# Optimization experiments

Hardware: AMD Instinct MI355X
Metric: run time of the kernel (lower is better)

## Reference

```python
import jax, jax.numpy as jnp
import numpy as np

TOP_K = 128
HID = 256


def _mlp2(h, w1, b1, w2, b2):
    return jax.nn.relu(h @ w1 + b1) @ w2 + b2


def setup_inputs() -> dict:
    key = jax.random.key(0)
    ks = jax.random.split(key, 20)
    B, L, D = 512, 256, 64
    s = 0.05
    inp = {
        "x": jax.random.normal(ks[0], (B, L, D), dtype=jnp.float32),
        "Wq": jax.random.normal(ks[1], (D, HID)) * s, "bq": jnp.zeros((HID,)),
        "Wk": jax.random.normal(ks[2], (D, HID)) * s, "bk": jnp.zeros((HID,)),
        "phi_w1": jax.random.normal(ks[3], (D, HID)) * s, "phi_b1": jnp.zeros((HID,)),
        "phi_w2": jax.random.normal(ks[4], (HID, HID)) * s, "phi_b2": jnp.zeros((HID,)),
        "xi_w1": jax.random.normal(ks[5], (2 * D, HID)) * s, "xi_b1": jnp.zeros((HID,)),
        "xi_w2": jax.random.normal(ks[6], (HID, HID)) * s, "xi_b2": jnp.zeros((HID,)),
        "rho_w1": jax.random.normal(ks[7], (HID, HID)) * s, "rho_b1": jnp.zeros((HID,)),
        "rho_w2": jax.random.normal(ks[8], (HID, 128)) * s, "rho_b2": jnp.zeros((128,)),
    }
    return inp


def reference(x, Wq, bq, Wk, bk, phi_w1, phi_b1, phi_w2, phi_b2,
              xi_w1, xi_b1, xi_w2, xi_b2, rho_w1, rho_b1, rho_w2, rho_b2):
    B, L, D = x.shape
    scale = HID ** (-0.5)
    # padding mask (all True for randn input; trim is identity with static shapes)
    pad = jnp.sum(jnp.abs(x), axis=-1) != 0  # [B, L]
    Q = x @ Wq + bq  # [B, L, H]
    K = x @ Wk + bk
    scores = jnp.einsum("blh,bmh->blm", Q, K) * scale  # [B, L, L]
    mask2d = pad[:, :, None] & pad[:, None, :]
    scores = jnp.where(mask2d, scores, -jnp.inf)
    flat = scores.reshape(B, L * L)
    k = min(TOP_K, L * L)
    topk_vals, topk_idx = jax.lax.top_k(flat, k)  # [B, k]
    topk_w = jax.nn.softmax(topk_vals, axis=-1)
    row = topk_idx // L
    col = topk_idx % L
    x_i = jnp.take_along_axis(x, row[:, :, None], axis=1)  # [B, k, D]
    x_j = jnp.take_along_axis(x, col[:, :, None], axis=1)
    feat_self = _mlp2(x_i, phi_w1, phi_b1, phi_w2, phi_b2)  # [B, k, H]
    feat_pair = _mlp2(jnp.concatenate([x_i, x_j], axis=-1), xi_w1, xi_b1, xi_w2, xi_b2)
    self_mask = (row == col)[:, :, None]
    interaction = jnp.where(self_mask, feat_self, feat_pair)
    pooled = jnp.sum(interaction * topk_w[:, :, None], axis=1)  # [B, H]
    return _mlp2(pooled, rho_w1, rho_b1, rho_w2, rho_b2)  # [B, 128]
```

## Files before the change

kernel.cpp:

```cpp
#include <hip/hip_runtime.h>

typedef unsigned short u16;
typedef unsigned int   u32;
typedef unsigned char  u8;
typedef unsigned long long u64;

#define B_TOT 512
#define L_SEQ 256
#define D_IN  64
#define HIDN  256
#define TOPK  128
#define CAP   160
#define NWT   32
#define FLDS  113280

typedef float  f32x4  __attribute__((ext_vector_type(4)));
typedef __bf16 bf16x8 __attribute__((ext_vector_type(8)));

__device__ __forceinline__ u16 f2bf(float f){
  u32 u = __float_as_uint(f);
  u32 r = u + 0x7fffu + ((u>>16)&1u);
  return (u16)(r>>16);
}
__device__ __forceinline__ u32 sortKey(float f){
  u32 b = __float_as_uint(f);
  return (b & 0x80000000u) ? ~b : (b | 0x80000000u);
}
__device__ __forceinline__ float unKey(u32 u){
  u32 b = (u & 0x80000000u) ? (u & 0x7fffffffu) : ~u;
  return __uint_as_float(b);
}
__device__ __forceinline__ void cvt8(const float* v, u32* hp, u32* lp){
  #pragma unroll
  for (int i=0;i<4;++i){
    float v0 = v[2*i], v1 = v[2*i+1];
    u16 h0 = f2bf(v0); float h0f = __uint_as_float(((u32)h0)<<16); u16 l0 = f2bf(v0 - h0f);
    u16 h1 = f2bf(v1); float h1f = __uint_as_float(((u32)h1)<<16); u16 l1 = f2bf(v1 - h1f);
    hp[i] = (u32)h0 | ((u32)h1<<16);
    lp[i] = (u32)l0 | ((u32)l1<<16);
  }
}

__global__ __launch_bounds__(256) void k_wprep(
    const float* __restrict__ Wq, const float* __restrict__ bq,
    const float* __restrict__ Wk, const float* __restrict__ bk,
    const float* __restrict__ xi_w1, const float* __restrict__ phi_w1,
    u16* __restrict__ MtH, u16* __restrict__ MtL, float* __restrict__ uvc,
    u16* __restrict__ xiH, u16* __restrict__ xiL,
    u16* __restrict__ phiH, u16* __restrict__ phiL)
{
  int bid = blockIdx.x, tid = threadIdx.x;
  if (bid < 64){
    __shared__ float wq[HIDN];
    __shared__ float part[256];
    int a = bid;
    wq[tid] = Wq[a*HIDN + tid];
    __syncthreads();
    int bcol = tid & 63, q = tid >> 6;
    float s = 0.f;
    for (int h = q*64; h < q*64 + 64; ++h)
      s = fmaf(wq[h], Wk[bcol*HIDN + h], s);
    part[tid] = s;
    __syncthreads();
    if (tid < 64){
      float mv = part[tid] + part[64+tid] + part[128+tid] + part[192+tid];
      u16 hh = f2bf(mv); float hf = __uint_as_float(((u32)hh)<<16);
      u16 ll = f2bf(mv - hf);
      MtH[tid*64 + a] = hh;
      MtL[tid*64 + a] = ll;
    }
    int wv = tid >> 6, ln = tid & 63;
    if (wv == 0){
      float s2 = 0.f;
      #pragma unroll
      for (int i=0;i<4;++i){ int h = ln*4+i; s2 = fmaf(wq[h], bk[h], s2); }
      #pragma unroll
      for (int off=1; off<64; off<<=1) s2 += __shfl_xor(s2, off);
      if (ln == 0) uvc[a] = s2;
    } else if (wv == 1){
      float s2 = 0.f;
      #pragma unroll
      for (int i=0;i<4;++i){ int h = ln*4+i; s2 = fmaf(Wk[a*HIDN + h], bq[h], s2); }
      #pragma unroll
      for (int off=1; off<64; off<<=1) s2 += __shfl_xor(s2, off);
      if (ln == 0) uvc[64 + a] = s2;
    } else if (wv == 2 && a == 0){
      float s2 = 0.f;
      #pragma unroll
      for (int i=0;i<4;++i){ int h = ln*4+i; s2 = fmaf(bq[h], bk[h], s2); }
      #pragma unroll
      for (int off=1; off<64; off<<=1) s2 += __shfl_xor(s2, off);
      if (ln == 0) uvc[128] = s2;
    }
  } else {
    int t = (bid-64)*256 + tid;
    if (t < 256*128){
      int h = t >> 7, d = t & 127;
      float v = xi_w1[d*HIDN + h];
      u16 hh = f2bf(v); float hf = __uint_as_float(((u32)hh)<<16);
      u16 ll = f2bf(v - hf);
      xiH[h*128 + d] = hh; xiL[h*128 + d] = ll;
    } else {
      int t2 = t - 256*128;
      int h = t2 >> 6, d = t2 & 63;
      float v = phi_w1[d*HIDN + h];
      u16 hh = f2bf(v); float hf = __uint_as_float(((u32)hh)<<16);
      u16 ll = f2bf(v - hf);
      phiH[h*64 + d] = hh; phiL[h*64 + d] = ll;
    }
  }
}

__global__ __launch_bounds__(512) void k_fused(
    const float* __restrict__ x, const u16* __restrict__ MtH, const u16* __restrict__ MtL,
    const float* __restrict__ uvc,
    u64* __restrict__ cand, int* __restrict__ cand_n)
{
  extern __shared__ __align__(16) u16 smem[];
  u16* XH = smem;
  u16* XL = XH + 256*72;
  u16* YH = XL + 256*72;
  u16* YL = YH + 128*72;
  float* STS = (float*)(YL + 128*72);
  float* STT = STS + 256;
  float* SUV = STT + 256;

  int tid = threadIdx.x;
  int b = blockIdx.x;
  const float* xb = x + (size_t)b*(L_SEQ*D_IN);

  if (tid < 129) SUV[tid] = uvc[tid];

  int ar = tid >> 1, ahf = tid & 1;
  float v[32];
  {
    const float* src = xb + (size_t)ar*D_IN + ahf*32;
    #pragma unroll
    for (int i=0;i<8;++i) *(float4*)&v[i*4] = *(const float4*)(src + i*4);
    u32 hp[16], lp[16];
    cvt8(&v[0],  &hp[0],  &lp[0]);
    cvt8(&v[8],  &hp[4],  &lp[4]);
    cvt8(&v[16], &hp[8],  &lp[8]);
    cvt8(&v[24], &hp[12], &lp[12]);
    u16* dh = XH + ar*72 + ahf*32;
    u16* dl = XL + ar*72 + ahf*32;
    #pragma unroll
    for (int i=0;i<4;++i){
      *(uint4*)(dh + i*8) = make_uint4(hp[i*4],hp[i*4+1],hp[i*4+2],hp[i*4+3]);
      *(uint4*)(dl + i*8) = make_uint4(lp[i*4],lp[i*4+1],lp[i*4+2],lp[i*4+3]);
    }
  }
  __syncthreads();

  {
    float pA=0.f, pB=0.f, qA=0.f, qB=0.f, pa=0.f;
    #pragma unroll
    for (int d=0; d<16; ++d){
      float xa = v[d];
      pA = fmaf(xa, SUV[ahf*32+d], pA);
      qA = fmaf(xa, SUV[64+ahf*32+d], qA);
      pa += fabsf(xa);
    }
    #pragma unroll
    for (int d=16; d<32; ++d){
      float xa = v[d];
      pB = fmaf(xa, SUV[ahf*32+d], pB);
      qB = fmaf(xa, SUV[64+ahf*32+d], qB);
      pa += fabsf(xa);
    }
    float su = pA + pB, tv = qA + qB;
    su += __shfl_xor(su,1); tv += __shfl_xor(tv,1); pa += __shfl_xor(pa,1);
    if (ahf == 0){
      bool pad = (pa != 0.f);
      STS[ar] = pad ? (su + SUV[128]) : -1e38f;
      STT[ar] = pad ? tv : -1e38f;
    }
  }
  __syncthreads();

  int w = tid >> 6, lane = tid & 63, lm = lane & 15, quad = lane >> 4;

  for (int half=0; half<2; ++half){
    int u = w + 8*half;
    int r0 = u*16;

    {
      const u16* ah = XH + (r0+lm)*72;
      const u16* al = XL + (r0+lm)*72;
      bf16x8 Ah0 = *(const bf16x8*)(ah + quad*8);
      bf16x8 Ah1 = *(const bf16x8*)(ah + 32 + quad*8);
      bf16x8 Al0 = *(const bf16x8*)(al + quad*8);
      bf16x8 Al1 = *(const bf16x8*)(al + 32 + quad*8);
      #pragma unroll
      for (int ct=0; ct<4; ++ct){
        const u16* mth = MtH + (ct*16+lm)*64 + quad*8;
        const u16* mtl = MtL + (ct*16+lm)*64 + quad*8;
        bf16x8 Bh0 = *(const bf16x8*)(mth);
        bf16x8 Bh1 = *(const bf16x8*)(mth + 32);
        bf16x8 Bl0 = *(const bf16x8*)(mtl);
        bf16x8 Bl1 = *(const bf16x8*)(mtl + 32);
        f32x4 a1 = {0.f,0.f,0.f,0.f}, a2 = {0.f,0.f,0.f,0.f};
        a1 = __builtin_amdgcn_mfma_f32_16x16x32_bf16(Ah0, Bh0, a1, 0,0,0);
        a2 = __builtin_amdgcn_mfma_f32_16x16x32_bf16(Ah1, Bh1, a2, 0,0,0);
        a1 = __builtin_amdgcn_mfma_f32_16x16x32_bf16(Al0, Bh0, a1, 0,0,0);
        a2 = __builtin_amdgcn_mfma_f32_16x16x32_bf16(Al1, Bh1, a2, 0,0,0);
        a1 = __builtin_amdgcn_mfma_f32_16x16x32_bf16(Ah0, Bl0, a1, 0,0,0);
        a2 = __builtin_amdgcn_mfma_f32_16x16x32_bf16(Ah1, Bl1, a2, 0,0,0);
        #pragma unroll
        for (int rg=0; rg<4; ++rg){
          float vy = a1[rg] + a2[rg];
          u16 hh = f2bf(vy); float hf = __uint_as_float(((u32)hh)<<16);
          u16 ll = f2bf(vy - hf);
          YH[(w*16 + quad*4 + rg)*72 + ct*16 + lm] = hh;
          YL[(w*16 + quad*4 + rg)*72 + ct*16 + lm] = ll;
        }
      }
    }
    const u16* yh_ = YH + (w*16+lm)*72;
    const u16* yl_ = YL + (w*16+lm)*72;
    bf16x8 Yh0 = *(const bf16x8*)(yh_ + quad*8);
    bf16x8 Yh1 = *(const bf16x8*)(yh_ + 32 + quad*8);
    bf16x8 Yl0 = *(const bf16x8*)(yl_ + quad*8);
    bf16x8 Yl1 = *(const bf16x8*)(yl_ + 32 + quad*8);

    float sr[4];
    #pragma unroll
    for (int r=0;r<4;++r) sr[r] = STS[r0 + quad*4 + r];

    for (int ch=0; ch<2; ++ch){
      int j0 = ch*128;
      u32 kv[32];
      #pragma unroll
      for (int ct=0; ct<8; ++ct){
        const u16* bh = XH + (j0 + ct*16+lm)*72;
        const u16* bl = XL + (j0 + ct*16+lm)*72;
        bf16x8 Bh0 = *(const bf16x8*)(bh + quad*8);
        bf16x8 Bh1 = *(const bf16x8*)(bh + 32 + quad*8);
        bf16x8 Bl0 = *(const bf16x8*)(bl + quad*8);
        bf16x8 Bl1 = *(const bf16x8*)(bl + 32 + quad*8);
        f32x4 a1 = {0.f,0.f,0.f,0.f}, a2 = {0.f,0.f,0.f,0.f};
        a1 = __builtin_amdgcn_mfma_f32_16x16x32_bf16(Yh0, Bh0, a1, 0,0,0);
        a2 = __builtin_amdgcn_mfma_f32_16x16x32_bf16(Yh1, Bh1, a2, 0,0,0);
        a1 = __builtin_amdgcn_mfma_f32_16x16x32_bf16(Yl0, Bh0, a1, 0,0,0);
        a2 = __builtin_amdgcn_mfma_f32_16x16x32_bf16(Yl1, Bh1, a2, 0,0,0);
        a1 = __builtin_amdgcn_mfma_f32_16x16x32_bf16(Yh0, Bl0, a1, 0,0,0);
        a2 = __builtin_amdgcn_mfma_f32_16x16x32_bf16(Yh1, Bl1, a2, 0,0,0);
        float tc = STT[j0 + ct*16 + lm];
        #pragma unroll
        for (int r=0;r<4;++r)
          kv[ct*4 + r] = sortKey(a1[r] + a2[r] + sr[r] + tc);
      }

      u32 T = 0;
      for (int bit=15; bit>=0; --bit){
        u32 th2 = (T | (1u<<bit)) << 16;
        int c = 0;
        #pragma unroll
        for (int i=0;i<32;++i)
          c += (int)__popcll(__ballot(kv[i] >= th2));
        if (c >= TOPK){
          T |= (1u<<bit);
          if (c <= CAP) break;
        }
      }
      u32 thr = T << 16;
      u32 up  = (T < 0xffffu) ? ((T+1u) << 16) : 0xffffffffu;

      u32 m1 = 0, m2 = 0;
      #pragma unroll
      for (int i=0;i<32;++i){
        bool ge = kv[i] >= thr;
        bool c1 = ge && (kv[i] >= up);
        m1 |= (c1 ? 1u : 0u) << i;
        m2 |= ((ge && !c1) ? 1u : 0u) << i;
      }
      int n1 = __popc(m1), n2 = __popc(m2);
      int p1 = n1, p2 = n2;
      #pragma unroll
      for (int off=1; off<64; off<<=1){
        int a = __shfl_up(p1, off); if (lane >= off) p1 += a;
        int c = __shfl_up(p2, off); if (lane >= off) p2 += c;
      }
      int tot1 = __shfl(p1, 63), tot2 = __shfl(p2, 63);
      int pos1 = p1 - n1;
      int pos2 = tot1 + (p2 - n2);
      int total = tot1 + tot2;
      int wt = u*2 + ch;
      size_t base = ((size_t)b*NWT + wt)*CAP;
      if (lane == 0) cand_n[b*NWT + wt] = (total < CAP) ? total : CAP;
      while (m1){
        int i = __ffs(m1) - 1; m1 &= m1 - 1;
        if (pos1 < CAP){
          int r = i & 3, ct = i >> 2;
          int flat = (r0 + quad*4 + r)*L_SEQ + (j0 + ct*16 + lm);
          cand[base + pos1] = ((u64)kv[i] << 32) | (u32)flat;
        }
        ++pos1;
      }
      while (m2){
        int i = __ffs(m2) - 1; m2 &= m2 - 1;
        if (pos2 < CAP){
          int r = i & 3, ct = i >> 2;
          int flat = (r0 + quad*4 + r)*L_SEQ + (j0 + ct*16 + lm);
          cand[base + pos2] = ((u64)kv[i] << 32) | (u32)flat;
        }
        ++pos2;
      }
    }
  }
}

__global__ __launch_bounds__(256) void k_pre(
    const float* __restrict__ x, const u16* __restrict__ MtH, const u16* __restrict__ MtL,
    const float* __restrict__ uvc,
    u16* __restrict__ xh, u16* __restrict__ xl,
    u16* __restrict__ yh, u16* __restrict__ yl,
    float* __restrict__ st)
{
  __shared__ __align__(16) u16 sh[64][72];
  __shared__ __align__(16) u16 sl[64][72];
  __shared__ float sUV[132];
  int tid = threadIdx.x;
  int g0 = blockIdx.x * 64;
  int b  = g0 >> 8, l0 = g0 & 255;
  int r = tid >> 2, q = tid & 3;

  if (tid < 129) sUV[tid] = uvc[tid];

  float v[16];
  {
    const float* xr = x + (size_t)(g0 + r)*D_IN + q*16;
    #pragma unroll
    for (int i=0;i<4;++i) *(float4*)&v[i*4] = *(const float4*)(xr + i*4);
  }
  {
    u32 hpA[4],lpA[4],hpB[4],lpB[4];
    cvt8(&v[0], hpA, lpA); cvt8(&v[8], hpB, lpB);
    size_t xo = (size_t)(g0 + r)*D_IN + q*16;
    *(uint4*)(xh + xo)     = make_uint4(hpA[0],hpA[1],hpA[2],hpA[3]);
    *(uint4*)(xh + xo + 8) = make_uint4(hpB[0],hpB[1],hpB[2],hpB[3]);
    *(uint4*)(xl + xo)     = make_uint4(lpA[0],lpA[1],lpA[2],lpA[3]);
    *(uint4*)(xl + xo + 8) = make_uint4(lpB[0],lpB[1],lpB[2],lpB[3]);
    *(uint4*)&sh[r][q*16]   = make_uint4(hpA[0],hpA[1],hpA[2],hpA[3]);
    *(uint4*)&sh[r][q*16+8] = make_uint4(hpB[0],hpB[1],hpB[2],hpB[3]);
    *(uint4*)&sl[r][q*16]   = make_uint4(lpA[0],lpA[1],lpA[2],lpA[3]);
    *(uint4*)&sl[r][q*16+8] = make_uint4(lpB[0],lpB[1],lpB[2],lpB[3]);
  }
  __syncthreads();

  {
    float su=0.f, tv=0.f, pa=0.f;
    #pragma unroll
    for (int d=0; d<16; ++d){
      float xa = v[d];
      su = fmaf(xa, sUV[q*16+d], su);
      tv = fmaf(xa, sUV[64+q*16+d], tv);
      pa += fabsf(xa);
    }
    su += __shfl_xor(su,1); su += __shfl_xor(su,2);
    tv += __shfl_xor(tv,1); tv += __shfl_xor(tv,2);
    pa += __shfl_xor(pa,1); pa += __shfl_xor(pa,2);
    if (q == 0){
      bool pad = (pa != 0.f);
      st[(size_t)b*L_SEQ + l0 + r]          = pad ? (su + sUV[128]) : -1e38f;
      st[(size_t)(B_TOT+b)*L_SEQ + l0 + r]  = pad ? tv : -1e38f;
    }
  }

  int w = tid >> 6, lane = tid & 63, lm = lane & 15, quad = lane >> 4;
  bf16x8 Ah0 = *(const bf16x8*)&sh[w*16+lm][quad*8];
  bf16x8 Ah1 = *(const bf16x8*)&sh[w*16+lm][32 + quad*8];
  bf16x8 Al0 = *(const bf16x8*)&sl[w*16+lm][quad*8];
  bf16x8 Al1 = *(const bf16x8*)&sl[w*16+lm][32 + quad*8];
  #pragma unroll
  for (int ct=0; ct<4; ++ct){
    const u16* mth = MtH + (ct*16+lm)*64 + quad*8;
    const u16* mtl = MtL + (ct*16+lm)*64 + quad*8;
    bf16x8 Bh0 = *(const bf16x8*)(mth);
    bf16x8 Bh1 = *(const bf16x8*)(mth + 32);
    bf16x8 Bl0 = *(const bf16x8*)(mtl);
    bf16x8 Bl1 = *(const bf16x8*)(mtl + 32);
    f32x4 a1 = {0.f,0.f,0.f,0.f}, a2 = {0.f,0.f,0.f,0.f};
    a1 = __builtin_amdgcn_mfma_f32_16x16x32_bf16(Ah0, Bh0, a1, 0,0,0);
    a2 = __builtin_amdgcn_mfma_f32_16x16x32_bf16(Ah1, Bh1, a2, 0,0,0);
    a1 = __builtin_amdgcn_mfma_f32_16x16x32_bf16(Al0, Bh0, a1, 0,0,0);
    a2 = __builtin_amdgcn_mfma_f32_16x16x32_bf16(Al1, Bh1, a2, 0,0,0);
    a1 = __builtin_amdgcn_mfma_f32_16x16x32_bf16(Ah0, Bl0, a1, 0,0,0);
    a2 = __builtin_amdgcn_mfma_f32_16x16x32_bf16(Ah1, Bl1, a2, 0,0,0);
    #pragma unroll
    for (int rg=0; rg<4; ++rg){
      float vy = a1[rg] + a2[rg];
      u16 hh = f2bf(vy); float hf = __uint_as_float(((u32)hh)<<16);
      u16 ll = f2bf(vy - hf);
      sh[w*16 + quad*4 + rg][ct*16 + lm] = hh;
      sl[w*16 + quad*4 + rg][ct*16 + lm] = ll;
    }
  }
  {
    size_t yo = (size_t)(g0 + r)*D_IN + q*16;
    *(uint4*)(yh + yo)     = *(uint4*)&sh[r][q*16];
    *(uint4*)(yh + yo + 8) = *(uint4*)&sh[r][q*16+8];
    *(uint4*)(yl + yo)     = *(uint4*)&sl[r][q*16];
    *(uint4*)(yl + yo + 8) = *(uint4*)&sl[r][q*16+8];
  }
}

__global__ __launch_bounds__(256) void k_score(
    const u16* __restrict__ xh, const u16* __restrict__ xl,
    const u16* __restrict__ yh, const u16* __restrict__ yl,
    const float* __restrict__ st,
    u64* __restrict__ cand, int* __restrict__ cand_n)
{
  int tid = threadIdx.x;
  int lin = blockIdx.x;
  int b    = ((lin >> 6) << 3) | (lin & 7);
  int tile = (lin >> 3) & 7;
  int cb = tile & 1, rb = tile >> 1;
  int r0 = rb*64, j0 = cb*128;
  int w = tid >> 6, lane = tid & 63, lm = lane & 15, quad = lane >> 4;

  size_t rowA = ((size_t)b*L_SEQ + r0 + w*16 + lm)*D_IN;
  bf16x8 A_h0 = *(const bf16x8*)(yh + rowA + quad*8);
  bf16x8 A_h1 = *(const bf16x8*)(yh + rowA + 32 + quad*8);
  bf16x8 A_l0 = *(const bf16x8*)(yl + rowA + quad*8);
  bf16x8 A_l1 = *(const bf16x8*)(yl + rowA + 32 + quad*8);

  float4 s4 = *(const float4*)(st + (size_t)b*L_SEQ + r0 + w*16 + quad*4);
  float sr[4] = {s4.x, s4.y, s4.z, s4.w};
  float tc[8];
  #pragma unroll
  for (int ct=0;ct<8;++ct)
    tc[ct] = st[(size_t)(B_TOT + b)*L_SEQ + j0 + ct*16 + lm];

  u32 kv[32];
  #pragma unroll
  for (int ct=0; ct<8; ++ct){
    size_t rowB = ((size_t)b*L_SEQ + j0 + ct*16 + lm)*D_IN;
    bf16x8 B_h0 = *(const bf16x8*)(xh + rowB + quad*8);
    bf16x8 B_h1 = *(const bf16x8*)(xh + rowB + 32 + quad*8);
    bf16x8 B_l0 = *(const bf16x8*)(xl + rowB + quad*8);
    bf16x8 B_l1 = *(const bf16x8*)(xl + rowB + 32 + quad*8);
    f32x4 a1 = {0.f,0.f,0.f,0.f}, a2 = {0.f,0.f,0.f,0.f};
    a1 = __builtin_amdgcn_mfma_f32_16x16x32_bf16(A_h0, B_h0, a1, 0,0,0);
    a2 = __builtin_amdgcn_mfma_f32_16x16x32_bf16(A_h1, B_h1, a2, 0,0,0);
    a1 = __builtin_amdgcn_mfma_f32_16x16x32_bf16(A_l0, B_h0, a1, 0,0,0);
    a2 = __builtin_amdgcn_mfma_f32_16x16x32_bf16(A_l1, B_h1, a2, 0,0,0);
    a1 = __builtin_amdgcn_mfma_f32_16x16x32_bf16(A_h0, B_l0, a1, 0,0,0);
    a2 = __builtin_amdgcn_mfma_f32_16x16x32_bf16(A_h1, B_l1, a2, 0,0,0);
    #pragma unroll
    for (int r=0;r<4;++r)
      kv[ct*4 + r] = sortKey(a1[r] + a2[r] + sr[r] + tc[ct]);
  }

  u32 T = 0;
  for (int bit=15; bit>=0; --bit){
    u32 th2 = (T | (1u<<bit)) << 16;
    int c = 0;
    #pragma unroll
    for (int i=0;i<32;++i)
      c += (int)__popcll(__ballot(kv[i] >= th2));
    if (c >= TOPK){
      T |= (1u<<bit);
      if (c <= CAP) break;
    }
  }
  u32 thr = T << 16;

  u32 hm = 0;
  #pragma unroll
  for (int i=0;i<32;++i) hm |= (kv[i] >= thr ? 1u : 0u) << i;
  int myc = __popc(hm);
  int pre = myc;
  #pragma unroll
  for (int off=1; off<64; off<<=1){
    int n = __shfl_up(pre, off);
    if (lane >= off) pre += n;
  }
  int total = __shfl(pre, 63);
  int pos = pre - myc;
  int wt = tile*4 + w;
  size_t base = ((size_t)b*NWT + wt)*CAP;
  if (lane == 0) cand_n[b*NWT + wt] = (total < CAP) ? total : CAP;
  while (hm){
    int i = __ffs(hm) - 1; hm &= hm - 1;
    if (pos < CAP){
      int r = i & 3, ct = i >> 2;
      int flat = (r0 + w*16 + quad*4 + r)*L_SEQ + (j0 + ct*16 + lm);
      cand[base + pos] = ((u64)kv[i] << 32) | (u32)flat;
    }
    ++pos;
  }
}

__global__ __launch_bounds__(256) void k_merge(
    const u64* __restrict__ cand, const int* __restrict__ cand_n,
    int* __restrict__ selidx, float* __restrict__ selw)
{
  const int SL   = NWT/4;
  const int NSW  = SL*CAP/64;
  const int WCAP = 192;
  __shared__ u64 wbuf[4][WCAP];
  __shared__ int wcnt[4];
  __shared__ int scnt[NWT];
  __shared__ int cm, eqc;
  __shared__ int eqi[256];
  __shared__ float sv[TOPK]; __shared__ int si[TOPK];
  __shared__ float fred[8];
  int b = blockIdx.x, tid = threadIdx.x;
  int w = tid >> 6, lane = tid & 63;
  if (tid < NWT) scnt[tid] = cand_n[b*NWT + tid];
  if (tid == 0){ cm = 0; eqc = 0; }
  __syncthreads();

  u32 key[NSW]; int idx[NSW];
  size_t bb = (size_t)b*NWT*CAP + (size_t)(w*SL)*CAP;
  #pragma unroll
  for (int s=0;s<NSW;++s){
    int e = lane + 64*s;
    int slot = e / CAP, p = e - slot*CAP;
    bool ok = p < scnt[w*SL + slot];
    u64 v = ok ? cand[bb + e] : 0ull;
    key[s] = (u32)(v >> 32);
    idx[s] = ok ? (int)(u32)v : 0x7fffffff;
  }

  u32 T = 0;
  for (int bit=31; bit>=0; --bit){
    u32 c2 = T | (1u<<bit);
    int c = 0;
    #pragma unroll
    for (int s=0;s<NSW;++s) c += (int)__popcll(__ballot(key[s] >= c2));
    if (c >= TOPK){
      T = c2;
      if (c <= WCAP) break;
    }
  }
  {
    int myc = 0;
    #pragma unroll
    for (int s=0;s<NSW;++s) myc += (key[s] >= T) ? 1 : 0;
    int pre = myc;
    #pragma unroll
    for (int off=1; off<64; off<<=1){
      int n = __shfl_up(pre, off);
      if (lane >= off) pre += n;
    }
    int total = __shfl(pre, 63);
    int pos = pre - myc;
    if (lane == 0) wcnt[w] = (total < WCAP) ? total : WCAP;
    #pragma unroll
    for (int s=0;s<NSW;++s){
      if (key[s] >= T){
        if (pos < WCAP) wbuf[w][pos] = ((u64)key[s] << 32) | (u32)idx[s];
        ++pos;
      }
    }
  }
  __syncthreads();

  if (w == 0){
    const int NS2 = 4*WCAP/64;
    u32 k2[NS2]; int i2[NS2];
    #pragma unroll
    for (int s=0;s<NS2;++s){
      int e = lane + 64*s;
      int slot = e / WCAP, p = e - slot*WCAP;
      bool ok = p < wcnt[slot];
      u64 v = ok ? wbuf[slot][p] : 0ull;
      k2[s] = (u32)(v >> 32);
      i2[s] = ok ? (int)(u32)v : 0x7fffffff;
    }
    u32 T2 = 0;
    for (int bit=31; bit>=0; --bit){
      u32 c2 = T2 | (1u<<bit);
      int c = 0;
      #pragma unroll
      for (int s=0;s<NS2;++s) c += (int)__popcll(__ballot(k2[s] >= c2));
      if (c >= TOPK) T2 = c2;
    }
    int m = 0;
    #pragma unroll
    for (int s=0;s<NS2;++s) m += (int)__popcll(__ballot(k2[s] > T2));
    #pragma unroll
    for (int s=0;s<NS2;++s){
      if (k2[s] > T2){
        int p = atomicAdd(&cm, 1);
        sv[p] = unKey(k2[s]) * 0.0625f; si[p] = i2[s];
      } else if (k2[s] == T2 && i2[s] != 0x7fffffff){
        int q = atomicAdd(&eqc, 1);
        if (q < 256) eqi[q] = i2[s];
      }
    }
    if (lane == 0){
      int need = TOPK - m;
      int n = eqc < 256 ? eqc : 256;
      float tv = unKey(T2) * 0.0625f;
      for (int s2=0; s2<need; ++s2){
        int bi = s2;
        for (int j=s2+1;j<n;++j) if (eqi[j] < eqi[bi]) bi = j;
        int t2 = eqi[s2]; eqi[s2] = eqi[bi]; eqi[bi] = t2;
        sv[m+s2] = tv; si[m+s2] = eqi[s2];
      }
    }
  }
  __syncthreads();

  float v = (tid < TOPK) ? sv[tid] : -3.4e38f;
  float mx = v;
  #pragma unroll
  for (int off=1; off<64; off<<=1) mx = fmaxf(mx, __shfl_xor(mx, off));
  if ((tid&63)==0) fred[tid>>6] = mx;
  __syncthreads();
  mx = fmaxf(fred[0], fred[1]);
  float e = (tid < TOPK) ? expf(v - mx) : 0.f;
  float s = e;
  #pragma unroll
  for (int off=1; off<64; off<<=1) s += __shfl_xor(s, off);
  if ((tid&63)==0) fred[4 + (tid>>6)] = s;
  __syncthreads();
  s = fred[4] + fred[5];
  if (tid < TOPK){
    selw[(size_t)b*TOPK + tid]   = e / s;
    selidx[(size_t)b*TOPK + tid] = si[tid];
  }
}

__global__ __launch_bounds__(256) void k_mlp(
    const float* __restrict__ x, const int* __restrict__ selidx, const float* __restrict__ selw,
    const u16* __restrict__ xiH, const u16* __restrict__ xiL,
    const u16* __restrict__ phiH, const u16* __restrict__ phiL,
    const float* __restrict__ phi_b1, const float* __restrict__ phi_w2, const float* __restrict__ phi_b2,
    const float* __restrict__ xi_b1,  const float* __restrict__ xi_w2,  const float* __restrict__ xi_b2,
    const float* __restrict__ rho_w1, const float* __restrict__ rho_b1,
    const float* __restrict__ rho_w2, const float* __restrict__ rho_b2,
    float* __restrict__ out)
{
  __shared__ __align__(16) u16 AFh[8][4][64][8];
  __shared__ __align__(16) u16 AFl[8][4][64][8];
  __shared__ int   sidx[TOPK];
  __shared__ float swp[TOPK], swd[TOPK];
  __shared__ float gpL[256], gsL[256];
  __shared__ float pooled[256], t1[256];
  __shared__ float wsums[2];
  int b = blockIdx.x, tid = threadIdx.x;

  if (tid < TOPK){
    int fl = selidx[(size_t)b*TOPK + tid];
    sidx[tid] = fl;
    float wv = selw[(size_t)b*TOPK + tid];
    bool dg = ((fl>>8) == (fl&255));
    swp[tid] = dg ? 0.f : wv;
    swd[tid] = dg ? wv  : 0.f;
  }
  __syncthreads();
  if (tid == 0){
    float a=0.f, c2=0.f;
    for (int k=0;k<TOPK;++k){ a+=swp[k]; c2+=swd[k]; }
    wsums[0]=a; wsums[1]=c2;
  }
  {
    int m = tid >> 1, hf = tid & 1;
    int fl = sidx[m];
    int rc = hf ? (fl & 255) : (fl >> 8);
    const float* src = x + ((size_t)b*L_SEQ + rc)*D_IN;
    int kt = m >> 4, l16 = m & 15;
    #pragma unroll
    for (int g=0; g<8; ++g){
      int d0 = hf*64 + g*8;
      int c = d0 >> 5, q = (d0 >> 3) & 3;
      float v[8];
      *(float4*)&v[0] = *(const float4*)(src + (d0 & 63));
      *(float4*)&v[4] = *(const float4*)(src + (d0 & 63) + 4);
      u32 hp[4], lp[4];
      cvt8(v, hp, lp);
      *(uint4*)&AFh[kt][c][l16 + 16*q][0] = make_uint4(hp[0],hp[1],hp[2],hp[3]);
      *(uint4*)&AFl[kt][c][l16 + 16*q][0] = make_uint4(lp[0],lp[1],lp[2],lp[3]);
    }
  }
  __syncthreads();

  int w = tid >> 6, lane = tid & 63;
  int lm = lane & 15, quad = lane >> 4;

  #pragma unroll
  for (int hi4=0; hi4<4; ++hi4){
    int ht = w + 4*hi4;
    int h  = ht*16 + lm;
    bf16x8 BXh[4], BXl[4], BPh[2], BPl[2];
    #pragma unroll
    for (int c=0;c<4;++c){
      BXh[c] = *(const bf16x8*)(xiH + h*128 + c*32 + quad*8);
      BXl[c] = *(const bf16x8*)(xiL + h*128 + c*32 + quad*8);
    }
    #pragma unroll
    for (int c=0;c<2;++c){
      BPh[c] = *(const bf16x8*)(phiH + h*64 + c*32 + quad*8);
      BPl[c] = *(const bf16x8*)(phiL + h*64 + c*32 + quad*8);
    }
    float bxi = xi_b1[h], bph = phi_b1[h];
    float gp = 0.f, gs = 0.f;
    for (int kt=0; kt<8; ++kt){
      bf16x8 Ah_[4], Al_[4];
      #pragma unroll
      for (int c=0;c<4;++c){
        Ah_[c] = *(const bf16x8*)&AFh[kt][c][lane][0];
        Al_[c] = *(const bf16x8*)&AFl[kt][c][lane][0];
      }
      f32x4 cx = {0.f,0.f,0.f,0.f}, cp = {0.f,0.f,0.f,0.f};
      #pragma unroll
      for (int c=0;c<4;++c){
        cx = __builtin_amdgcn_mfma_f32_16x16x32_bf16(Ah_[c], BXh[c], cx, 0,0,0);
        cx = __builtin_amdgcn_mfma_f32_16x16x32_bf16(Al_[c], BXh[c], cx, 0,0,0);
        cx = __builtin_amdgcn_mfma_f32_16x16x32_bf16(Ah_[c], BXl[c], cx, 0,0,0);
      }
      #pragma unroll
      for (int c=0;c<2;++c){
        cp = __builtin_amdgcn_mfma_f32_16x16x32_bf16(Ah_[c], BPh[c], cp, 0,0,0);
        cp = __builtin_amdgcn_mfma_f32_16x16x32_bf16(Al_[c], BPh[c], cp, 0,0,0);
        cp = __builtin_amdgcn_mfma_f32_16x16x32_bf16(Ah_[c], BPl[c], cp, 0,0,0);
      }
      #pragma unroll
      for (int r=0;r<4;++r){
        int kk = kt*16 + quad*4 + r;
        gp = fmaf(swp[kk], fmaxf(cx[r] + bxi, 0.f), gp);
        gs = fmaf(swd[kk], fmaxf(cp[r] + bph, 0.f), gs);
      }
    }
    gp += __shfl_xor(gp, 16); gp += __shfl_xor(gp, 32);
    gs += __shfl_xor(gs, 16); gs += __shfl_xor(gs, 32);
    if (quad == 0){ gpL[h] = gp; gsL[h] = gs; }
  }
  __syncthreads();

  int h = tid;
  {
    float wsp = wsums[0], wss = wsums[1];
    float po = wsp*xi_b2[h] + wss*phi_b2[h];
    for (int d=0; d<256; ++d){
      po = fmaf(gpL[d], xi_w2[d*HIDN + h], po);
      po = fmaf(gsL[d], phi_w2[d*HIDN + h], po);
    }
    pooled[h] = po;
  }
  __syncthreads();
  {
    float a = rho_b1[h];
    for (int d=0; d<256; ++d) a = fmaf(pooled[d], rho_w1[d*HIDN + h], a);
    t1[h] = fmaxf(a, 0.f);
  }
  __syncthreads();
  if (h < 128){
    float o = rho_b2[h];
    for (int d=0; d<256; ++d) o = fmaf(t1[d], rho_w2[d*128 + h], o);
    out[(size_t)b*128 + h] = o;
  }
}

extern "C" void kernel_launch(void* const* d_in, const int* in_sizes, int n_in,
                              void* d_out, int out_size, void* d_ws, size_t ws_size,
                              hipStream_t stream)
{
  (void)in_sizes; (void)n_in; (void)out_size; (void)ws_size;
  const float* x      = (const float*)d_in[0];
  const float* Wq     = (const float*)d_in[1];
  const float* bq     = (const float*)d_in[2];
  const float* Wk     = (const float*)d_in[3];
  const float* bk     = (const float*)d_in[4];
  const float* phi_w1 = (const float*)d_in[5];
  const float* phi_b1 = (const float*)d_in[6];
  const float* phi_w2 = (const float*)d_in[7];
  const float* phi_b2 = (const float*)d_in[8];
  const float* xi_w1  = (const float*)d_in[9];
  const float* xi_b1  = (const float*)d_in[10];
  const float* xi_w2  = (const float*)d_in[11];
  const float* xi_b2  = (const float*)d_in[12];
  const float* rho_w1 = (const float*)d_in[13];
  const float* rho_b1 = (const float*)d_in[14];
  const float* rho_w2 = (const float*)d_in[15];
  const float* rho_b2 = (const float*)d_in[16];
  float* out = (float*)d_out;

  const size_t NX = (size_t)B_TOT*L_SEQ*D_IN;
  float* uvc    = (float*)d_ws;
  float* st     = uvc + 256;
  float* selw   = st + (size_t)2*B_TOT*L_SEQ;
  int*   selidx = (int*)(selw + (size_t)B_TOT*TOPK);
  int*   cand_n = selidx + (size_t)B_TOT*TOPK;
  u64*   cand   = (u64*)(cand_n + (size_t)B_TOT*NWT);
  u16*   MtH    = (u16*)(cand + (size_t)B_TOT*NWT*CAP);
  u16*   MtL    = MtH + 64*64;
  u16*   xiH    = MtL + 64*64;
  u16*   xiL    = xiH + 256*128;
  u16*   phiH   = xiL + 256*128;
  u16*   phiL   = phiH + 256*64;
  u16*   xh     = phiL + 256*64;
  u16*   xl     = xh + NX;
  u16*   yh     = xl + NX;
  u16*   yl     = yh + NX;

  hipError_t aerr = hipFuncSetAttribute((const void*)k_fused,
                      hipFuncAttributeMaxDynamicSharedMemorySize, FLDS);

  k_wprep<<<dim3(256),  dim3(256), 0, stream>>>(Wq, bq, Wk, bk, xi_w1, phi_w1,
                                                MtH, MtL, uvc, xiH, xiL, phiH, phiL);
  if (aerr == hipSuccess){
    k_fused<<<dim3(B_TOT), dim3(512), FLDS, stream>>>(x, MtH, MtL, uvc, cand, cand_n);
  } else {
    k_pre  <<<dim3(2048), dim3(256), 0, stream>>>(x, MtH, MtL, uvc, xh, xl, yh, yl, st);
    k_score<<<dim3(4096), dim3(256), 0, stream>>>(xh, xl, yh, yl, st, cand, cand_n);
  }
  k_merge<<<dim3(B_TOT), dim3(256), 0, stream>>>(cand, cand_n, selidx, selw);
  k_mlp  <<<dim3(B_TOT), dim3(256), 0, stream>>>(x, selidx, selw,
            xiH, xiL, phiH, phiL,
            phi_b1, phi_w2, phi_b2,
            xi_b1, xi_w2, xi_b2,
            rho_w1, rho_b1, rho_w2, rho_b2, out);
}
```

Baseline: 271.7 us.

## Interleave dual-chunk top-k selection and pass per-tile thresholds to seed merge search

The fused scoring kernel now computes both 128-column chunks up front and runs their radix threshold searches, prefix scans and candidate writes interleaved. This raises instruction-level parallelism and replaces the serial ffs loops with unrolled predicated stores. Each tile's threshold is written to a new workspace array. The merge kernel uses the maximum of these as a lower bound, skipping radix bits already known to be set in both of its selection stages. Holding two 32-entry key arrays at once raises register pressure.

After: 335.0 us. 23.3% more time.

```diff
diff --git a/kernel.cpp b/kernel.cpp
--- a/kernel.cpp
+++ b/kernel.cpp
@@ -114,7 +114,7 @@
 __global__ __launch_bounds__(512) void k_fused(
     const float* __restrict__ x, const u16* __restrict__ MtH, const u16* __restrict__ MtL,
     const float* __restrict__ uvc,
-    u64* __restrict__ cand, int* __restrict__ cand_n)
+    u64* __restrict__ cand, int* __restrict__ cand_n, u32* __restrict__ uthr)
 {
   extern __shared__ __align__(16) u16 smem[];
   u16* XH = smem;
@@ -227,84 +227,124 @@
     #pragma unroll
     for (int r=0;r<4;++r) sr[r] = STS[r0 + quad*4 + r];
 
-    for (int ch=0; ch<2; ++ch){
-      int j0 = ch*128;
-      u32 kv[32];
-      #pragma unroll
-      for (int ct=0; ct<8; ++ct){
-        const u16* bh = XH + (j0 + ct*16+lm)*72;
-        const u16* bl = XL + (j0 + ct*16+lm)*72;
-        bf16x8 Bh0 = *(const bf16x8*)(bh + quad*8);
-        bf16x8 Bh1 = *(const bf16x8*)(bh + 32 + quad*8);
-        bf16x8 Bl0 = *(const bf16x8*)(bl + quad*8);
-        bf16x8 Bl1 = *(const bf16x8*)(bl + 32 + quad*8);
-        f32x4 a1 = {0.f,0.f,0.f,0.f}, a2 = {0.f,0.f,0.f,0.f};
-        a1 = __builtin_amdgcn_mfma_f32_16x16x32_bf16(Yh0, Bh0, a1, 0,0,0);
-        a2 = __builtin_amdgcn_mfma_f32_16x16x32_bf16(Yh1, Bh1, a2, 0,0,0);
-        a1 = __builtin_amdgcn_mfma_f32_16x16x32_bf16(Yl0, Bh0, a1, 0,0,0);
-        a2 = __builtin_amdgcn_mfma_f32_16x16x32_bf16(Yl1, Bh1, a2, 0,0,0);
-        a1 = __builtin_amdgcn_mfma_f32_16x16x32_bf16(Yh0, Bl0, a1, 0,0,0);
-        a2 = __builtin_amdgcn_mfma_f32_16x16x32_bf16(Yh1, Bl1, a2, 0,0,0);
-        float tc = STT[j0 + ct*16 + lm];
-        #pragma unroll
-        for (int r=0;r<4;++r)
-          kv[ct*4 + r] = sortKey(a1[r] + a2[r] + sr[r] + tc);
-      }
-
-      u32 T = 0;
-      for (int bit=15; bit>=0; --bit){
-        u32 th2 = (T | (1u<<bit)) << 16;
-        int c = 0;
-        #pragma unroll
-        for (int i=0;i<32;++i)
-          c += (int)__popcll(__ballot(kv[i] >= th2));
-        if (c >= TOPK){
-          T |= (1u<<bit);
-          if (c <= CAP) break;
+    u32 kvA[32], kvB[32];
+    #pragma unroll
+    for (int ct=0; ct<8; ++ct){
+      const u16* bh = XH + (ct*16+lm)*72;
+      const u16* bl = XL + (ct*16+lm)*72;
+      bf16x8 Bh0 = *(const bf16x8*)(bh + quad*8);
+      bf16x8 Bh1 = *(const bf16x8*)(bh + 32 + quad*8);
+      bf16x8 Bl0 = *(const bf16x8*)(bl + quad*8);
+      bf16x8 Bl1 = *(const bf16x8*)(bl + 32 + quad*8);
+      f32x4 a1 = {0.f,0.f,0.f,0.f}, a2 = {0.f,0.f,0.f,0.f};
+      a1 = __builtin_amdgcn_mfma_f32_16x16x32_bf16(Yh0, Bh0, a1, 0,0,0);
+      a2 = __builtin_amdgcn_mfma_f32_16x16x32_bf16(Yh1, Bh1, a2, 0,0,0);
+      a1 = __builtin_amdgcn_mfma_f32_16x16x32_bf16(Yl0, Bh0, a1, 0,0,0);
+      a2 = __builtin_amdgcn_mfma_f32_16x16x32_bf16(Yl1, Bh1, a2, 0,0,0);
+      a1 = __builtin_amdgcn_mfma_f32_16x16x32_bf16(Yh0, Bl0, a1, 0,0,0);
+      a2 = __builtin_amdgcn_mfma_f32_16x16x32_bf16(Yh1, Bl1, a2, 0,0,0);
+      float tc = STT[ct*16 + lm];
+      #pragma unroll
+      for (int r=0;r<4;++r)
+        kvA[ct*4 + r] = sortKey(a1[r] + a2[r] + sr[r] + tc);
+    }
+    #pragma unroll
+    for (int ct=0; ct<8; ++ct){
+      const u16* bh = XH + (128 + ct*16+lm)*72;
+      const u16* bl = XL + (128 + ct*16+lm)*72;
+      bf16x8 Bh0 = *(const bf16x8*)(bh + quad*8);
+      bf16x8 Bh1 = *(const bf16x8*)(bh + 32 + quad*8);
+      bf16x8 Bl0 = *(const bf16x8*)(bl + quad*8);
+      bf16x8 Bl1 = *(const bf16x8*)(bl + 32 + quad*8);
+      f32x4 a1 = {0.f,0.f,0.f,0.f}, a2 = {0.f,0.f,0.f,0.f};
+      a1 = __builtin_amdgcn_mfma_f32_16x16x32_bf16(Yh0, Bh0, a1, 0,0,0);
+      a2 = __builtin_amdgcn_mfma_f32_16x16x32_bf16(Yh1, Bh1, a2, 0,0,0);
+      a1 = __builtin_amdgcn_mfma_f32_16x16x32_bf16(Yl0, Bh0, a1, 0,0,0);
+      a2 = __builtin_amdgcn_mfma_f32_16x16x32_bf16(Yl1, Bh1, a2, 0,0,0);
+      a1 = __builtin_amdgcn_mfma_f32_16x16x32_bf16(Yh0, Bl0, a1, 0,0,0);
+      a2 = __builtin_amdgcn_mfma_f32_16x16x32_bf16(Yh1, Bl1, a2, 0,0,0);
+      float tc = STT[128 + ct*16 + lm];
+      #pragma unroll
+      for (int r=0;r<4;++r)
+        kvB[ct*4 + r] = sortKey(a1[r] + a2[r] + sr[r] + tc);
+    }
+
+    u32 TA = 0, TB = 0; int dA = 0, dB = 0;
+    for (int bit=15; bit>=0; --bit){
+      u32 msk = 1u << bit;
+      u32 thA = (TA | msk) << 16;
+      u32 thB = (TB | msk) << 16;
+      int cA = 0, cB = 0;
+      #pragma unroll
+      for (int i=0;i<32;++i){
+        cA += (int)__popcll(__ballot(kvA[i] >= thA));
+        cB += (int)__popcll(__ballot(kvB[i] >= thB));
+      }
+      if (!dA && cA >= TOPK){ TA |= msk; dA = (cA <= CAP); }
+      if (!dB && cB >= TOPK){ TB |= msk; dB = (cB <= CAP); }
+      if (dA & dB) break;
+    }
+
+    u32 thrA = TA << 16, thrB = TB << 16;
+    u32 upA  = (TA < 0xffffu) ? ((TA+1u) << 16) : 0xffffffffu;
+    u32 upB  = (TB < 0xffffu) ? ((TB+1u) << 16) : 0xffffffffu;
+
+    u32 m1A=0,m2A=0,m1B=0,m2B=0;
+    #pragma unroll
+    for (int i=0;i<32;++i){
+      bool gA = kvA[i] >= thrA, hA = kvA[i] >= upA;
+      m1A |= (hA ? 1u : 0u) << i;
+      m2A |= ((gA && !hA) ? 1u : 0u) << i;
+      bool gB = kvB[i] >= thrB, hB = kvB[i] >= upB;
+      m1B |= (hB ? 1u : 0u) << i;
+      m2B |= ((gB && !hB) ? 1u : 0u) << i;
+    }
+    int n1A=__popc(m1A), n2A=__popc(m2A), n1B=__popc(m1B), n2B=__popc(m2B);
+    int p1A=n1A, p2A=n2A, p1B=n1B, p2B=n2B;
+    #pragma unroll
+    for (int off=1; off<64; off<<=1){
+      int aa=__shfl_up(p1A,off), bb2=__shfl_up(p2A,off);
+      int cc=__shfl_up(p1B,off), dd=__shfl_up(p2B,off);
+      if (lane >= off){ p1A+=aa; p2A+=bb2; p1B+=cc; p2B+=dd; }
+    }
+    int tot1A=__shfl(p1A,63), tot2A=__shfl(p2A,63);
+    int tot1B=__shfl(p1B,63), tot2B=__shfl(p2B,63);
+    int pos1A = p1A - n1A, pos2A = tot1A + (p2A - n2A);
+    int pos1B = p1B - n1B, pos2B = tot1B + (p2B - n2B);
+    int wtA = u*2, wtB = u*2 + 1;
+    size_t baseA = ((size_t)b*NWT + wtA)*CAP;
+    size_t baseB = ((size_t)b*NWT + wtB)*CAP;
+    if (lane == 0){
+      int ta = tot1A + tot2A, tb2 = tot1B + tot2B;
+      cand_n[b*NWT + wtA] = (ta  < CAP) ? ta  : CAP;
+      cand_n[b*NWT + wtB] = (tb2 < CAP) ? tb2 : CAP;
+      uthr[b*NWT + wtA] = thrA;
+      uthr[b*NWT + wtB] = thrB;
+    }
+    {
+      int o1=0, o2=0;
+      #pragma unroll
+      for (int i=0;i<32;++i){
+        bool c1 = (m1A >> i) & 1u, c2v = (m2A >> i) & 1u;
+        if (c1 | c2v){
+          int p = c1 ? (pos1A + o1) : (pos2A + o2);
+          int flat = (r0 + quad*4 + (i&3))*L_SEQ + ((i>>2)*16 + lm);
+          if (p < CAP) cand[baseA + p] = ((u64)kvA[i] << 32) | (u32)flat;
         }
-      }
-      u32 thr = T << 16;
-      u32 up  = (T < 0xffffu) ? ((T+1u) << 16) : 0xffffffffu;
-
-      u32 m1 = 0, m2 = 0;
+        o1 += c1; o2 += c2v;
+      }
+    }
+    {
+      int o1=0, o2=0;
       #pragma unroll
       for (int i=0;i<32;++i){
-        bool ge = kv[i] >= thr;
-        bool c1 = ge && (kv[i] >= up);
-        m1 |= (c1 ? 1u : 0u) << i;
-        m2 |= ((ge && !c1) ? 1u : 0u) << i;
-      }
-      int n1 = __popc(m1), n2 = __popc(m2);
-      int p1 = n1, p2 = n2;
-      #pragma unroll
-      for (int off=1; off<64; off<<=1){
-        int a = __shfl_up(p1, off); if (lane >= off) p1 += a;
-        int c = __shfl_up(p2, off); if (lane >= off) p2 += c;
-      }
-      int tot1 = __shfl(p1, 63), tot2 = __shfl(p2, 63);
-      int pos1 = p1 - n1;
-      int pos2 = tot1 + (p2 - n2);
-      int total = tot1 + tot2;
-      int wt = u*2 + ch;
-      size_t base = ((size_t)b*NWT + wt)*CAP;
-      if (lane == 0) cand_n[b*NWT + wt] = (total < CAP) ? total : CAP;
-      while (m1){
-        int i = __ffs(m1) - 1; m1 &= m1 - 1;
-        if (pos1 < CAP){
-          int r = i & 3, ct = i >> 2;
-          int flat = (r0 + quad*4 + r)*L_SEQ + (j0 + ct*16 + lm);
-          cand[base + pos1] = ((u64)kv[i] << 32) | (u32)flat;
+        bool c1 = (m1B >> i) & 1u, c2v = (m2B >> i) & 1u;
+        if (c1 | c2v){
+          int p = c1 ? (pos1B + o1) : (pos2B + o2);
+          int flat = (r0 + quad*4 + (i&3))*L_SEQ + (128 + (i>>2)*16 + lm);
+          if (p < CAP) cand[baseB + p] = ((u64)kvB[i] << 32) | (u32)flat;
         }
-        ++pos1;
-      }
-      while (m2){
-        int i = __ffs(m2) - 1; m2 &= m2 - 1;
-        if (pos2 < CAP){
-          int r = i & 3, ct = i >> 2;
-          int flat = (r0 + quad*4 + r)*L_SEQ + (j0 + ct*16 + lm);
-          cand[base + pos2] = ((u64)kv[i] << 32) | (u32)flat;
-        }
-        ++pos2;
+        o1 += c1; o2 += c2v;
       }
     }
   }
@@ -409,7 +449,7 @@
     const u16* __restrict__ xh, const u16* __restrict__ xl,
     const u16* __restrict__ yh, const u16* __restrict__ yl,
     const float* __restrict__ st,
-    u64* __restrict__ cand, int* __restrict__ cand_n)
+    u64* __restrict__ cand, int* __restrict__ cand_n, u32* __restrict__ uthr)
 {
   int tid = threadIdx.x;
   int lin = blockIdx.x;
@@ -480,7 +520,10 @@
   int pos = pre - myc;
   int wt = tile*4 + w;
   size_t base = ((size_t)b*NWT + wt)*CAP;
-  if (lane == 0) cand_n[b*NWT + wt] = (total < CAP) ? total : CAP;
+  if (lane == 0){
+    cand_n[b*NWT + wt] = (total < CAP) ? total : CAP;
+    uthr[b*NWT + wt] = thr;
+  }
   while (hm){
     int i = __ffs(hm) - 1; hm &= hm - 1;
     if (pos < CAP){
@@ -493,7 +536,7 @@
 }
 
 __global__ __launch_bounds__(256) void k_merge(
-    const u64* __restrict__ cand, const int* __restrict__ cand_n,
+    const u64* __restrict__ cand, const int* __restrict__ cand_n, const u32* __restrict__ uthr,
     int* __restrict__ selidx, float* __restrict__ selw)
 {
   const int SL   = NWT/4;
@@ -502,6 +545,7 @@
   __shared__ u64 wbuf[4][WCAP];
   __shared__ int wcnt[4];
   __shared__ int scnt[NWT];
+  __shared__ u32 wT[4];
   __shared__ int cm, eqc;
   __shared__ int eqi[256];
   __shared__ float sv[TOPK]; __shared__ int si[TOPK];
@@ -524,9 +568,17 @@
     idx[s] = ok ? (int)(u32)v : 0x7fffffff;
   }
 
+  u32 lb = uthr[b*NWT + w*SL + (lane & 7)];
+  #pragma unroll
+  for (int off=1; off<8; off<<=1){
+    u32 o = (u32)__shfl_xor((int)lb, off);
+    lb = lb > o ? lb : o;
+  }
+
   u32 T = 0;
   for (int bit=31; bit>=0; --bit){
     u32 c2 = T | (1u<<bit);
+    if (c2 <= lb){ T = c2; continue; }
     int c = 0;
     #pragma unroll
     for (int s=0;s<NSW;++s) c += (int)__popcll(__ballot(key[s] >= c2));
@@ -535,6 +587,7 @@
       if (c <= WCAP) break;
     }
   }
+  if (lane == 0) wT[w] = T;
   {
     int myc = 0;
     #pragma unroll
@@ -570,9 +623,14 @@
       k2[s] = (u32)(v >> 32);
       i2[s] = ok ? (int)(u32)v : 0x7fffffff;
     }
+    u32 lb2 = wT[0];
+    lb2 = lb2 > wT[1] ? lb2 : wT[1];
+    lb2 = lb2 > wT[2] ? lb2 : wT[2];
+    lb2 = lb2 > wT[3] ? lb2 : wT[3];
     u32 T2 = 0;
     for (int bit=31; bit>=0; --bit){
       u32 c2 = T2 | (1u<<bit);
+      if (c2 <= lb2){ T2 = c2; continue; }
       int c = 0;
       #pragma unroll
       for (int s=0;s<NS2;++s) c += (int)__popcll(__ballot(k2[s] >= c2));
@@ -786,7 +844,8 @@
   float* selw   = st + (size_t)2*B_TOT*L_SEQ;
   int*   selidx = (int*)(selw + (size_t)B_TOT*TOPK);
   int*   cand_n = selidx + (size_t)B_TOT*TOPK;
-  u64*   cand   = (u64*)(cand_n + (size_t)B_TOT*NWT);
+  u32*   uthr   = (u32*)(cand_n + (size_t)B_TOT*NWT);
+  u64*   cand   = (u64*)(uthr + (size_t)B_TOT*NWT);
   u16*   MtH    = (u16*)(cand + (size_t)B_TOT*NWT*CAP);
   u16*   MtL    = MtH + 64*64;
   u16*   xiH    = MtL + 64*64;
@@ -804,12 +863,12 @@
   k_wprep<<<dim3(256),  dim3(256), 0, stream>>>(Wq, bq, Wk, bk, xi_w1, phi_w1,
                                                 MtH, MtL, uvc, xiH, xiL, phiH, phiL);
   if (aerr == hipSuccess){
-    k_fused<<<dim3(B_TOT), dim3(512), FLDS, stream>>>(x, MtH, MtL, uvc, cand, cand_n);
+    k_fused<<<dim3(B_TOT), dim3(512), FLDS, stream>>>(x, MtH, MtL, uvc, cand, cand_n, uthr);
   } else {
     k_pre  <<<dim3(2048), dim3(256), 0, stream>>>(x, MtH, MtL, uvc, xh, xl, yh, yl, st);
-    k_score<<<dim3(4096), dim3(256), 0, stream>>>(xh, xl, yh, yl, st, cand, cand_n);
-  }
-  k_merge<<<dim3(B_TOT), dim3(256), 0, stream>>>(cand, cand_n, selidx, selw);
+    k_score<<<dim3(4096), dim3(256), 0, stream>>>(xh, xl, yh, yl, st, cand, cand_n, uthr);
+  }
+  k_merge<<<dim3(B_TOT), dim3(256), 0, stream>>>(cand, cand_n, uthr, selidx, selw);
   k_mlp  <<<dim3(B_TOT), dim3(256), 0, stream>>>(x, selidx, selw,
             xiH, xiL, phiH, phiL,
             phi_b1, phi_w2, phi_b2,
```
